# Kernel optimization log

Measured on AMD Instinct MI355X. Metric: run time of the kernel, lower is better.

Reference implementation:

```python
import jax, jax.numpy as jnp
import numpy as np

B, S, D = 4, 2048, 1024
H, DK, DV = 16, 64, 64


def setup_inputs() -> dict:
    key = jax.random.key(0)
    ks = jax.random.split(key, 12)
    sd = 0.02
    return {
        "input_query": jax.random.normal(ks[0], (B, S, D), jnp.float32),
        "input_key": jax.random.normal(ks[1], (B, S, D), jnp.float32),
        "input_value": jax.random.normal(ks[2], (B, S, D), jnp.float32),
        "Wq": jax.random.normal(ks[3], (H, D, DK), jnp.float32) * sd,
        "bq": jax.random.normal(ks[4], (H, DK), jnp.float32) * sd,
        "Wk": jax.random.normal(ks[5], (H, D, DK), jnp.float32) * sd,
        "bk": jax.random.normal(ks[6], (H, DK), jnp.float32) * sd,
        "Wv": jax.random.normal(ks[7], (H, D, DV), jnp.float32) * sd,
        "bv": jax.random.normal(ks[8], (H, DV), jnp.float32) * sd,
        "Wo": jax.random.normal(ks[9], (H * DV, D), jnp.float32) * sd,
        "bo": jax.random.normal(ks[10], (D,), jnp.float32) * sd,
    }


def reference(input_query, input_key, input_value, Wq, bq, Wk, bk, Wv, bv, Wo, bo):
    # per-head projections, batched over all heads at once
    q = jnp.einsum("bsd,hdk->bhsk", input_query, Wq) + bq[None, :, None, :]
    k = jnp.einsum("bsd,hdk->bhsk", input_key, Wk) + bk[None, :, None, :]
    v = jnp.einsum("bsd,hdv->bhsv", input_value, Wv) + bv[None, :, None, :]
    # NOTE: original code computes self.dk = sqrt(d_k) but never divides by it,
    # so scores are UNSCALED QK^T (faithful to the source).
    score = jnp.einsum("bhqk,bhsk->bhqs", q, k)  # [B,H,S,S]
    score = jax.nn.softmax(score, axis=-1)
    z = jnp.einsum("bhqs,bhsv->bhqv", score, v)  # [B,H,S,DV]
    # concat heads along feature dim (dim=2 in torch) -> [B,S,H*DV]
    z = jnp.transpose(z, (0, 2, 1, 3)).reshape(z.shape[0], z.shape[2], -1)
    return z @ Wo + bo
```

## Files before the change

### kernel.cpp

```cpp
#include <hip/hip_runtime.h>


using short8  = __attribute__((ext_vector_type(8))) short;
using short4_t= __attribute__((ext_vector_type(4))) short;
using floatx4 = __attribute__((ext_vector_type(4))) float;

#define MFMA32(a, b, c) __builtin_amdgcn_mfma_f32_16x16x32_bf16((a), (b), (c), 0, 0, 0)
#define MFMA16(a, b, c) __builtin_amdgcn_mfma_f32_16x16x16bf16_1k((a), (b), (c), 0, 0, 0)

__device__ __forceinline__ void async16(const unsigned short* g, unsigned short* lds_base) {
  __builtin_amdgcn_global_load_lds(
      (const __attribute__((address_space(1))) unsigned int*)g,
      (__attribute__((address_space(3))) unsigned int*)lds_base, 16, 0, 0);
}

__device__ __forceinline__ float bf2f(unsigned short u) {
  union { unsigned int i; float f; } v; v.i = ((unsigned int)u) << 16; return v.f;
}
__device__ __forceinline__ unsigned short f2bf(float f) {
  union { float f; unsigned int i; } v; v.f = f;
  unsigned int r = v.i + 0x7FFFu + ((v.i >> 16) & 1u);
  return (unsigned short)(r >> 16);
}
__device__ __forceinline__ unsigned int fbits(float f) {
  union { float f; unsigned int i; } v; v.f = f; return v.i;
}
__device__ __forceinline__ unsigned short ld_bf(const void* p, size_t idx, int isbf16) {
  return isbf16 ? ((const unsigned short*)p)[idx] : f2bf(((const float*)p)[idx]);
}
__device__ __forceinline__ float ld_f(const void* p, size_t idx, int isbf16) {
  return isbf16 ? bf2f(((const unsigned short*)p)[idx]) : ((const float*)p)[idx];
}

__global__ void detect_dtype(const unsigned int* __restrict__ X,
                             unsigned int* __restrict__ flag) {
  __shared__ int red[256];
  int cnt = 0;
  for (int i = threadIdx.x; i < 4096; i += 256) {
    unsigned int e = (X[i] >> 7) & 0xFFu;
    cnt += (e >= 96u && e <= 160u) ? 1 : 0;
  }
  red[threadIdx.x] = cnt;
  __syncthreads();
  for (int s = 128; s > 0; s >>= 1) {
    if (threadIdx.x < (unsigned)s) red[threadIdx.x] += red[threadIdx.x + s];
    __syncthreads();
  }
  if (threadIdx.x == 0) *flag = (red[0] >= 2560) ? 1u : 0u;
}

__global__ void convert3(const void* __restrict__ X0, const void* __restrict__ X1,
                         const void* __restrict__ X2,
                         unsigned short* __restrict__ Y0, unsigned short* __restrict__ Y1,
                         unsigned short* __restrict__ Y2,
                         int n8, const unsigned int* __restrict__ flagp) {
  const int isbf16 = (int)*flagp;
  const int z = blockIdx.z;
  const void* X = (z == 0) ? X0 : (z == 1) ? X1 : X2;
  unsigned short* Y = (z == 0) ? Y0 : (z == 1) ? Y1 : Y2;
  int i = blockIdx.x * blockDim.x + threadIdx.x;
  if (i >= n8) return;
  if (isbf16) {
    ((uint4*)Y)[i] = ((const uint4*)X)[i];
  } else {
    const float* f = (const float*)X + (size_t)i * 8;
    union { unsigned short u[8]; uint4 v; } t;
#pragma unroll
    for (int j = 0; j < 8; ++j) t.u[j] = f2bf(f[j]);
    ((uint4*)Y)[i] = t.v;
  }
}

__global__ void transpose_w3(const void* __restrict__ W0, const void* __restrict__ W1,
                             const void* __restrict__ W2,
                             unsigned short* __restrict__ T,
                             const unsigned int* __restrict__ flagp) {
  const int isbf16 = (int)*flagp;
  __shared__ unsigned short tile[32][33];
  const int w = blockIdx.z >> 4, hh = blockIdx.z & 15;
  const void* in = (w == 0) ? W0 : (w == 1) ? W1 : W2;
  const size_t boff = (size_t)hh * 1024 * 64;
  unsigned short* op = T + (size_t)w * (1u << 20) + boff;
  const int r0 = blockIdx.y * 32, c0 = blockIdx.x * 32;
#pragma unroll
  for (int i = 0; i < 4; ++i) {
    int r = threadIdx.y + i * 8;
    tile[r][threadIdx.x] = ld_bf(in, boff + (size_t)(r0 + r) * 64 + (c0 + threadIdx.x), isbf16);
  }
  __syncthreads();
#pragma unroll
  for (int i = 0; i < 4; ++i) {
    int c = threadIdx.y + i * 8;
    op[(size_t)(c0 + c) * 1024 + (r0 + threadIdx.x)] = tile[threadIdx.x][c];
  }
}

__global__ void transpose_any(const void* __restrict__ in,
                              unsigned short* __restrict__ out,
                              int R, int C, const unsigned int* __restrict__ flagp) {
  const int isbf16 = (int)*flagp;
  __shared__ unsigned short tile[32][33];
  const int r0 = blockIdx.y * 32, c0 = blockIdx.x * 32;
#pragma unroll
  for (int i = 0; i < 4; ++i) {
    int r = threadIdx.y + i * 8;
    tile[r][threadIdx.x] = ld_bf(in, (size_t)(r0 + r) * C + (c0 + threadIdx.x), isbf16);
  }
  __syncthreads();
#pragma unroll
  for (int i = 0; i < 4; ++i) {
    int c = threadIdx.y + i * 8;
    out[(size_t)(c0 + c) * R + (r0 + threadIdx.x)] = tile[threadIdx.x][c];
  }
}

#define GEMM_MAIN_LOOP(Aq, Btq, Kdim)                                          \
  floatx4 acc[4][4];                                                           \
  _Pragma("unroll") for (int i = 0; i < 4; ++i)                                \
      _Pragma("unroll") for (int j = 0; j < 4; ++j)                            \
          acc[i][j] = (floatx4){0.f, 0.f, 0.f, 0.f};                           \
  const int lrow = lane >> 3, scol = (lane & 7) * 8;                           \
  for (int k0 = 0; k0 < (Kdim); k0 += 64) {                                    \
    __syncthreads();                                                           \
    _Pragma("unroll") for (int r = 0; r < 4; ++r) {                            \
      const int chunk = r * 4 + wave;                                          \
      const int row = chunk * 8 + lrow;                                        \
      async16(&(Aq)[(size_t)(m0 + row) * (Kdim) + k0 + scol],                  \
              &a_lds[(size_t)chunk * 512]);                                    \
      async16(&(Btq)[(size_t)(n0 + row) * (Kdim) + k0 + scol],                 \
              &b_lds[(size_t)chunk * 512]);                                    \
    }                                                                          \
    __syncthreads();                                                           \
    _Pragma("unroll") for (int kk = 0; kk < 2; ++kk) {                         \
      short8 af[4];                                                            \
      _Pragma("unroll") for (int i = 0; i < 4; ++i)                            \
          af[i] = *(const short8*)&a_lds[(wm + i * 16 + ln15) * 64 + kk * 32 + quad * 8]; \
      _Pragma("unroll") for (int j = 0; j < 4; ++j) {                          \
        short8 bf = *(const short8*)&b_lds[(wn + j * 16 + ln15) * 64 + kk * 32 + quad * 8]; \
        _Pragma("unroll") for (int i = 0; i < 4; ++i)                          \
            acc[i][j] = MFMA32(af[i], bf, acc[i][j]);                          \
      }                                                                        \
    }                                                                          \
  }

__global__ __launch_bounds__(256) void gemm_qkv(
    const unsigned short* __restrict__ A0, const unsigned short* __restrict__ A1,
    const unsigned short* __restrict__ A2,
    const unsigned short* __restrict__ BT,
    const void* __restrict__ b0, const void* __restrict__ b1,
    const void* __restrict__ b2,
    unsigned short* __restrict__ Qp, unsigned short* __restrict__ Kp,
    unsigned short* __restrict__ Vt,
    const unsigned int* __restrict__ flagp)
{
  const int isbf16 = (int)*flagp;
  const int z = blockIdx.z;
  const unsigned short* A  = (z == 0) ? A0 : (z == 1) ? A1 : A2;
  const unsigned short* Bt = BT + ((size_t)z << 20);
  const void* bias = (z == 0) ? b0 : (z == 1) ? b1 : b2;
  const int m0 = blockIdx.x * 128, n0 = blockIdx.y * 128;
  const int tid = threadIdx.x, wave = tid >> 6, lane = tid & 63;
  const int ln15 = lane & 15, quad = lane >> 4;
  const int wm = (wave >> 1) * 64, wn = (wave & 1) * 64;
  __shared__ alignas(16) unsigned short a_lds[128 * 64];
  __shared__ alignas(16) unsigned short b_lds[128 * 64];

  GEMM_MAIN_LOOP(A, Bt, 1024)

  if (z < 2) {
    unsigned short* C = z ? Kp : Qp;
#pragma unroll
    for (int j = 0; j < 4; ++j) {
      const int col = n0 + wn + j * 16 + ln15;
      const float bv = ld_f(bias, col, isbf16);
#pragma unroll
      for (int i = 0; i < 4; ++i) {
        const int row = m0 + wm + i * 16 + quad * 4;
#pragma unroll
        for (int r = 0; r < 4; ++r)
          C[(size_t)(row + r) * 1024 + col] = f2bf(acc[i][j][r] + bv);
      }
    }
  } else {
    __syncthreads();
#pragma unroll
    for (int j = 0; j < 4; ++j) {
      const int nl = wn + j * 16 + ln15;
      const float bv = ld_f(bias, n0 + nl, isbf16);
      unsigned short* dst = (nl < 64) ? &a_lds[(size_t)nl * 128]
                                      : &b_lds[(size_t)(nl - 64) * 128];
#pragma unroll
      for (int i = 0; i < 4; ++i) {
        const int ml = wm + i * 16 + quad * 4;
#pragma unroll
        for (int r = 0; r < 4; ++r) dst[ml + r] = f2bf(acc[i][j][r] + bv);
      }
    }
    __syncthreads();
    const int nl = tid >> 1, half = tid & 1;
    const unsigned short* src = (nl < 64) ? &a_lds[(size_t)nl * 128 + half * 64]
                                          : &b_lds[(size_t)(nl - 64) * 128 + half * 64];
    const int bb = m0 >> 11, s0 = m0 & 2047;
    unsigned short* dst = Vt + (size_t)bb * 2048 * 1024 +
                          (size_t)(n0 + nl) * 2048 + s0 + half * 64;
#pragma unroll
    for (int c = 0; c < 8; ++c) *(uint4*)&dst[c * 8] = *(const uint4*)&src[c * 8];
  }
}

__global__ __launch_bounds__(256) void gemm_out(
    const unsigned short* __restrict__ A,
    const unsigned short* __restrict__ Bt,
    const void* __restrict__ bias,
    void* __restrict__ C,
    const unsigned int* __restrict__ flagp)
{
  const int isbf16 = (int)*flagp;
  const int m0 = blockIdx.x * 128, n0 = blockIdx.y * 128;
  const int tid = threadIdx.x, wave = tid >> 6, lane = tid & 63;
  const int ln15 = lane & 15, quad = lane >> 4;
  const int wm = (wave >> 1) * 64, wn = (wave & 1) * 64;
  __shared__ alignas(16) unsigned short a_lds[128 * 64];
  __shared__ alignas(16) unsigned short b_lds[128 * 64];

  GEMM_MAIN_LOOP(A, Bt, 1024)

#pragma unroll
  for (int j = 0; j < 4; ++j) {
    const int col = n0 + wn + j * 16 + ln15;
    const float bv = ld_f(bias, col, isbf16);
#pragma unroll
    for (int i = 0; i < 4; ++i) {
      const int row = m0 + wm + i * 16 + quad * 4;
#pragma unroll
      for (int r = 0; r < 4; ++r) {
        const float val = acc[i][j][r] + bv;
        if (!isbf16) ((float*)C)[(size_t)(row + r) * 1024 + col] = val;
        else ((unsigned short*)C)[(size_t)(row + r) * 1024 + col] = f2bf(val);
      }
    }
  }
}

__global__ __launch_bounds__(256, 2) void attn(
    const unsigned short* __restrict__ Q,
    const unsigned short* __restrict__ K,
    const unsigned short* __restrict__ Vt,
    unsigned short* __restrict__ Z)
{
  const int qt0 = blockIdx.x * 256, h = blockIdx.y, b = blockIdx.z;
  const int tid = threadIdx.x, wave = tid >> 6, lane = tid & 63;
  const int ln15 = lane & 15, quad = lane >> 4;

  __shared__ alignas(16) char smem[55296];
  unsigned short* q_lds = (unsigned short*)smem;
  unsigned short* k_lds = (unsigned short*)(smem + 36864);
  unsigned short* v_lds = (unsigned short*)(smem + 46080);

  const unsigned short* Qb = Q + ((size_t)(b * 2048 + qt0)) * 1024 + h * 64;
  const unsigned short* Kb = K + ((size_t)(b * 2048)) * 1024 + h * 64;
  const unsigned short* Vh = Vt + (size_t)b * 2048 * 1024 + (size_t)h * 64 * 2048;

  const int sr = tid >> 2, sc = (tid & 3) * 16;
#pragma unroll
  for (int i = 0; i < 4; ++i) {
    const int r = sr + i * 64;
    *(uint4*)&q_lds[r * 72 + sc]     = *(const uint4*)&Qb[(size_t)r * 1024 + sc];
    *(uint4*)&q_lds[r * 72 + sc + 8] = *(const uint4*)&Qb[(size_t)r * 1024 + sc + 8];
  }
  __syncthreads();
  short8 qf[4][2];
#pragma unroll
  for (int g = 0; g < 4; ++g) {
    const int row = (g * 4 + wave) * 16 + ln15;
    qf[g][0] = *(const short8*)&q_lds[row * 72 + quad * 8];
    qf[g][1] = *(const short8*)&q_lds[row * 72 + 32 + quad * 8];
  }

  floatx4 o_acc[4][4];
#pragma unroll
  for (int g = 0; g < 4; ++g)
#pragma unroll
    for (int vb = 0; vb < 4; ++vb) o_acc[g][vb] = (floatx4){0.f, 0.f, 0.f, 0.f};
  float l_part[4] = {0.f, 0.f, 0.f, 0.f};

  for (int j0 = 0; j0 < 2048; j0 += 64) {
    __syncthreads();
    *(uint4*)&k_lds[sr * 72 + sc]     = *(const uint4*)&Kb[(size_t)(j0 + sr) * 1024 + sc];
    *(uint4*)&k_lds[sr * 72 + sc + 8] = *(const uint4*)&Kb[(size_t)(j0 + sr) * 1024 + sc + 8];
    *(uint4*)&v_lds[sr * 72 + sc]     = *(const uint4*)&Vh[(size_t)sr * 2048 + j0 + sc];
    *(uint4*)&v_lds[sr * 72 + sc + 8] = *(const uint4*)&Vh[(size_t)sr * 2048 + j0 + sc + 8];
    __syncthreads();

    short8 kf[4][2];
    short4_t vf[4][4];
#pragma unroll
    for (int nb = 0; nb < 4; ++nb) {
      kf[nb][0] = *(const short8*)&k_lds[(nb * 16 + ln15) * 72 + quad * 8];
      kf[nb][1] = *(const short8*)&k_lds[(nb * 16 + ln15) * 72 + 32 + quad * 8];
    }
#pragma unroll
    for (int vb = 0; vb < 4; ++vb)
#pragma unroll
      for (int nb = 0; nb < 4; ++nb)
        vf[vb][nb] = *(const short4_t*)&v_lds[(vb * 16 + ln15) * 72 + nb * 16 + quad * 4];

#pragma unroll
    for (int g = 0; g < 4; ++g) {
      short4_t pb[4];
#pragma unroll
      for (int nb = 0; nb < 4; ++nb) {
        floatx4 st = (floatx4){0.f, 0.f, 0.f, 0.f};
        st = MFMA32(kf[nb][0], qf[g][0], st);
        st = MFMA32(kf[nb][1], qf[g][1], st);
        const float p0 = __expf(st[0]), p1 = __expf(st[1]);
        const float p2 = __expf(st[2]), p3 = __expf(st[3]);
        l_part[g] += (p0 + p1) + (p2 + p3);
        union { unsigned int u[2]; short4_t s; } pk;
        pk.u[0] = (fbits(p0) >> 16) | (fbits(p1) & 0xFFFF0000u);
        pk.u[1] = (fbits(p2) >> 16) | (fbits(p3) & 0xFFFF0000u);
        pb[nb] = pk.s;
      }
#pragma unroll
      for (int vb = 0; vb < 4; ++vb)
#pragma unroll
        for (int nb = 0; nb < 4; ++nb)
          o_acc[g][vb] = MFMA16(vf[vb][nb], pb[nb], o_acc[g][vb]);
    }
  }

  __syncthreads();
  float* ot = (float*)smem;
  const int q = tid >> 2, vg = (tid & 3) * 16;
#pragma unroll
  for (int g = 0; g < 4; ++g) {
    float l = l_part[g];
    l += __shfl_xor(l, 16);
    l += __shfl_xor(l, 32);
    const float rl = 1.0f / l;
#pragma unroll
    for (int vb = 0; vb < 4; ++vb)
#pragma unroll
      for (int r = 0; r < 4; ++r)
        ot[(wave * 16 + ln15) * 66 + vb * 16 + quad * 4 + r] = o_acc[g][vb][r] * rl;
    __syncthreads();
    union { unsigned short u[16]; uint4 v[2]; } t;
#pragma unroll
    for (int i = 0; i < 16; ++i) t.u[i] = f2bf(ot[q * 66 + vg + i]);
    unsigned short* dst = Z + ((size_t)(b * 2048 + qt0 + g * 64 + q)) * 1024 + h * 64 + vg;
    *(uint4*)&dst[0] = t.v[0];
    *(uint4*)&dst[8] = t.v[1];
    __syncthreads();
  }
}

extern "C" void kernel_launch(void* const* d_in, const int* in_sizes, int n_in,
                              void* d_out, int out_size, void* d_ws, size_t ws_size,
                              hipStream_t stream) {
  const void* Xq = d_in[0];
  const void* Xk = d_in[1];
  const void* Xv = d_in[2];
  const void* Wq = d_in[3];
  const void* bq = d_in[4];
  const void* Wk = d_in[5];
  const void* bk = d_in[6];
  const void* Wv = d_in[7];
  const void* bv = d_in[8];
  const void* Wo = d_in[9];
  const void* bo = d_in[10];

  unsigned int*   flag = (unsigned int*)d_ws;
  unsigned short* base = (unsigned short*)d_ws + 128;
  unsigned short* WqT = base;
  unsigned short* WoT = WqT + (3u << 20);
  unsigned short* buf0 = WoT + (1u << 20);
  unsigned short* buf1 = buf0 + (8u << 20);
  unsigned short* buf2 = buf1 + (8u << 20);
  unsigned short* buf3 = buf2 + (8u << 20);
  unsigned short* buf4 = buf3 + (8u << 20);
  unsigned short* buf5 = buf4 + (8u << 20);
  unsigned short *Xqc = buf0, *Xkc = buf1, *Xvc = buf2;
  unsigned short *Qp = buf3, *Kp = buf4, *VtR = buf5;
  unsigned short *Zp = buf2;

  detect_dtype<<<1, 256, 0, stream>>>((const unsigned int*)Xq, flag);

  transpose_w3<<<dim3(2, 32, 48), dim3(32, 8), 0, stream>>>(Wq, Wk, Wv, WqT, flag);
  transpose_any<<<dim3(32, 32), dim3(32, 8), 0, stream>>>(Wo, WoT, 1024, 1024, flag);

  const int n8 = (8 << 20) / 8;
  convert3<<<dim3(n8 / 256, 1, 3), 256, 0, stream>>>(Xq, Xk, Xv, Xqc, Xkc, Xvc, n8, flag);

  gemm_qkv<<<dim3(64, 8, 3), 256, 0, stream>>>(Xqc, Xkc, Xvc, WqT, bq, bk, bv,
                                               Qp, Kp, VtR, flag);

  attn<<<dim3(8, 16, 4), 256, 0, stream>>>(Qp, Kp, VtR, Zp);

  gemm_out<<<dim3(64, 8), 256, 0, stream>>>(Zp, WoT, bo, d_out, flag);
}
```

Before: 370.6 us.

## Fuse conversion and weight transposes into one prep kernel; XOR-swizzle GEMM LDS

Merges the input fp32-to-bf16 conversion and the Wq/Wk/Wv and Wo transposes into a single launch that dispatches on block index, removing two kernel launches and their serialization gaps. Separately, the GEMM main loop now stores A/B tiles into LDS with an XOR swizzle on the 16-byte column group and reads back with the matching swizzle, to reduce LDS bank conflicts on the MFMA fragment loads. The fused kernel mixes heterogeneous block types, and the swizzle must stay consistent between the async store and the fragment reads.

```diff
diff --git a/kernel.cpp b/kernel.cpp
--- a/kernel.cpp
+++ b/kernel.cpp
@@ -49,68 +49,73 @@
   if (threadIdx.x == 0) *flag = (red[0] >= 2560) ? 1u : 0u;
 }
 
-__global__ void convert3(const void* __restrict__ X0, const void* __restrict__ X1,
-                         const void* __restrict__ X2,
-                         unsigned short* __restrict__ Y0, unsigned short* __restrict__ Y1,
-                         unsigned short* __restrict__ Y2,
-                         int n8, const unsigned int* __restrict__ flagp) {
+__global__ __launch_bounds__(256) void prep(
+    const void* __restrict__ Xq, const void* __restrict__ Xk,
+    const void* __restrict__ Xv,
+    const void* __restrict__ Wq, const void* __restrict__ Wk,
+    const void* __restrict__ Wv, const void* __restrict__ Wo,
+    unsigned short* __restrict__ Xqc, unsigned short* __restrict__ Xkc,
+    unsigned short* __restrict__ Xvc,
+    unsigned short* __restrict__ WT,
+    unsigned short* __restrict__ WoT,
+    const unsigned int* __restrict__ flagp)
+{
   const int isbf16 = (int)*flagp;
-  const int z = blockIdx.z;
-  const void* X = (z == 0) ? X0 : (z == 1) ? X1 : X2;
-  unsigned short* Y = (z == 0) ? Y0 : (z == 1) ? Y1 : Y2;
-  int i = blockIdx.x * blockDim.x + threadIdx.x;
-  if (i >= n8) return;
-  if (isbf16) {
-    ((uint4*)Y)[i] = ((const uint4*)X)[i];
+  const int bid = blockIdx.x, tid = threadIdx.x;
+
+  if (bid < 12288) {
+    const int z = bid >> 12;
+    const int i = ((bid & 4095) << 8) + tid;
+    const void* X = (z == 0) ? Xq : (z == 1) ? Xk : Xv;
+    unsigned short* Y = (z == 0) ? Xqc : (z == 1) ? Xkc : Xvc;
+    if (isbf16) {
+      ((uint4*)Y)[i] = ((const uint4*)X)[i];
+    } else {
+      const float* f = (const float*)X + (size_t)i * 8;
+      union { unsigned short u[8]; uint4 v; } t;
+#pragma unroll
+      for (int j = 0; j < 8; ++j) t.u[j] = f2bf(f[j]);
+      ((uint4*)Y)[i] = t.v;
+    }
+    return;
+  }
+
+  __shared__ unsigned short tile[32][33];
+  const int tx = tid & 31, ty = tid >> 5;
+  const int t = bid - 12288;
+  if (t < 3072) {
+    const int x = t & 1, y = (t >> 1) & 31, zz = t >> 6;
+    const int w = zz >> 4, hh = zz & 15;
+    const void* in = (w == 0) ? Wq : (w == 1) ? Wk : Wv;
+    const size_t boff = (size_t)hh * 1024 * 64;
+    unsigned short* op = WT + ((size_t)w << 20) + boff;
+    const int r0 = y * 32, c0 = x * 32;
+#pragma unroll
+    for (int i = 0; i < 4; ++i) {
+      int r = ty + i * 8;
+      tile[r][tx] = ld_bf(in, boff + (size_t)(r0 + r) * 64 + (c0 + tx), isbf16);
+    }
+    __syncthreads();
+#pragma unroll
+    for (int i = 0; i < 4; ++i) {
+      int c = ty + i * 8;
+      op[(size_t)(c0 + c) * 1024 + (r0 + tx)] = tile[tx][c];
+    }
   } else {
-    const float* f = (const float*)X + (size_t)i * 8;
-    union { unsigned short u[8]; uint4 v; } t;
-#pragma unroll
-    for (int j = 0; j < 8; ++j) t.u[j] = f2bf(f[j]);
-    ((uint4*)Y)[i] = t.v;
-  }
-}
-
-__global__ void transpose_w3(const void* __restrict__ W0, const void* __restrict__ W1,
-                             const void* __restrict__ W2,
-                             unsigned short* __restrict__ T,
-                             const unsigned int* __restrict__ flagp) {
-  const int isbf16 = (int)*flagp;
-  __shared__ unsigned short tile[32][33];
-  const int w = blockIdx.z >> 4, hh = blockIdx.z & 15;
-  const void* in = (w == 0) ? W0 : (w == 1) ? W1 : W2;
-  const size_t boff = (size_t)hh * 1024 * 64;
-  unsigned short* op = T + (size_t)w * (1u << 20) + boff;
-  const int r0 = blockIdx.y * 32, c0 = blockIdx.x * 32;
-#pragma unroll
-  for (int i = 0; i < 4; ++i) {
-    int r = threadIdx.y + i * 8;
-    tile[r][threadIdx.x] = ld_bf(in, boff + (size_t)(r0 + r) * 64 + (c0 + threadIdx.x), isbf16);
-  }
-  __syncthreads();
-#pragma unroll
-  for (int i = 0; i < 4; ++i) {
-    int c = threadIdx.y + i * 8;
-    op[(size_t)(c0 + c) * 1024 + (r0 + threadIdx.x)] = tile[threadIdx.x][c];
-  }
-}
-
-__global__ void transpose_any(const void* __restrict__ in,
-                              unsigned short* __restrict__ out,
-                              int R, int C, const unsigned int* __restrict__ flagp) {
-  const int isbf16 = (int)*flagp;
-  __shared__ unsigned short tile[32][33];
-  const int r0 = blockIdx.y * 32, c0 = blockIdx.x * 32;
-#pragma unroll
-  for (int i = 0; i < 4; ++i) {
-    int r = threadIdx.y + i * 8;
-    tile[r][threadIdx.x] = ld_bf(in, (size_t)(r0 + r) * C + (c0 + threadIdx.x), isbf16);
-  }
-  __syncthreads();
-#pragma unroll
-  for (int i = 0; i < 4; ++i) {
-    int c = threadIdx.y + i * 8;
-    out[(size_t)(c0 + c) * R + (r0 + threadIdx.x)] = tile[threadIdx.x][c];
+    const int t2 = t - 3072;
+    const int x = t2 & 31, y = t2 >> 5;
+    const int r0 = y * 32, c0 = x * 32;
+#pragma unroll
+    for (int i = 0; i < 4; ++i) {
+      int r = ty + i * 8;
+      tile[r][tx] = ld_bf(Wo, (size_t)(r0 + r) * 1024 + (c0 + tx), isbf16);
+    }
+    __syncthreads();
+#pragma unroll
+    for (int i = 0; i < 4; ++i) {
+      int c = ty + i * 8;
+      WoT[(size_t)(c0 + c) * 1024 + (r0 + tx)] = tile[tx][c];
+    }
   }
 }
 
@@ -119,7 +124,9 @@
   _Pragma("unroll") for (int i = 0; i < 4; ++i)                                \
       _Pragma("unroll") for (int j = 0; j < 4; ++j)                            \
           acc[i][j] = (floatx4){0.f, 0.f, 0.f, 0.f};                           \
-  const int lrow = lane >> 3, scol = (lane & 7) * 8;                           \
+  const int lrow = lane >> 3, cg = lane & 7;                                   \
+  const int scol = ((cg ^ lrow) * 8);                                          \
+  const int sw = ln15 & 7;                                                     \
   for (int k0 = 0; k0 < (Kdim); k0 += 64) {                                    \
     __syncthreads();                                                           \
     _Pragma("unroll") for (int r = 0; r < 4; ++r) {                            \
@@ -134,9 +141,11 @@
     _Pragma("unroll") for (int kk = 0; kk < 2; ++kk) {                         \
       short8 af[4];                                                            \
       _Pragma("unroll") for (int i = 0; i < 4; ++i)                            \
-          af[i] = *(const short8*)&a_lds[(wm + i * 16 + ln15) * 64 + kk * 32 + quad * 8]; \
+          af[i] = *(const short8*)&a_lds[(wm + i * 16 + ln15) * 64 +           \
+                                         (((kk * 4 + quad) ^ sw) * 8)];        \
       _Pragma("unroll") for (int j = 0; j < 4; ++j) {                          \
-        short8 bf = *(const short8*)&b_lds[(wn + j * 16 + ln15) * 64 + kk * 32 + quad * 8]; \
+        short8 bf = *(const short8*)&b_lds[(wn + j * 16 + ln15) * 64 +         \
+                                           (((kk * 4 + quad) ^ sw) * 8)];      \
         _Pragma("unroll") for (int i = 0; i < 4; ++i)                          \
             acc[i][j] = MFMA32(af[i], bf, acc[i][j]);                          \
       }                                                                        \
@@ -385,11 +394,8 @@
 
   detect_dtype<<<1, 256, 0, stream>>>((const unsigned int*)Xq, flag);
 
-  transpose_w3<<<dim3(2, 32, 48), dim3(32, 8), 0, stream>>>(Wq, Wk, Wv, WqT, flag);
-  transpose_any<<<dim3(32, 32), dim3(32, 8), 0, stream>>>(Wo, WoT, 1024, 1024, flag);
-
-  const int n8 = (8 << 20) / 8;
-  convert3<<<dim3(n8 / 256, 1, 3), 256, 0, stream>>>(Xq, Xk, Xv, Xqc, Xkc, Xvc, n8, flag);
+  prep<<<16384, 256, 0, stream>>>(Xq, Xk, Xv, Wq, Wk, Wv, Wo,
+                                  Xqc, Xkc, Xvc, WqT, WoT, flag);
 
   gemm_qkv<<<dim3(64, 8, 3), 256, 0, stream>>>(Xqc, Xkc, Xvc, WqT, bq, bk, bv,
                                                Qp, Kp, VtR, flag);
```

Measured after the change: 348.4 us. -6.0%, faster.
